# Kernel optimization log

Hardware: AMD Instinct MI355X
Metric: run time of the kernel (lower is better)

Reference implementation:

```python
import jax, jax.numpy as jnp
import numpy as np

TEMP_DIV = 13.0  # forward hard-codes attn / 13 (self.temperature is unused)


def setup_inputs() -> dict:
    key = jax.random.key(0)
    k1, k2, k3 = jax.random.split(key, 3)
    B, Lq, Lk, D = 8, 2048, 2048, 640
    q = jax.random.normal(k1, (B, Lq, D), dtype=jnp.float32)
    k = jax.random.normal(k2, (B, Lk, D), dtype=jnp.float32)
    v = jax.random.normal(k3, (B, Lk, D), dtype=jnp.float32)
    return {"q": q, "k": k, "v": v}


def _l2_scores(q, k):
    # -sum((q[:,:,None,:] - k[:,None,:,:])**2, axis=3) via the GEMM expansion
    # ||q||^2 - 2 q.k + ||k||^2  -> avoids the (B,Lq,Lk,D) intermediate.
    qq = jnp.sum(q * q, axis=-1)            # (B, Lq)
    kk = jnp.sum(k * k, axis=-1)            # (B, Lk)
    qk = jnp.einsum('bqd,bkd->bqk', q, k)   # (B, Lq, Lk)
    return -(qq[:, :, None] - 2.0 * qk + kk[:, None, :])


def reference(q, k, v):
    attn_logits = _l2_scores(q, k) / TEMP_DIV          # (B, Lq, Lk)
    log_attn = jax.nn.log_softmax(attn_logits, axis=2)
    attn = jnp.exp(log_attn)                            # softmax, shares the stable pass
    # dropout is identity in eval mode
    output = jnp.einsum('bqk,bkd->bqd', attn, v)        # bmm
    return (output, attn, log_attn)
```

## Files before the change

kernel.cpp:

```cpp
#include <hip/hip_runtime.h>


#define B_   8
#define LQ   2048
#define LK   2048
#define DD   640

typedef short s16x8 __attribute__((ext_vector_type(8)));
typedef float f32x4 __attribute__((ext_vector_type(4)));

__device__ __forceinline__ unsigned short f2bf(float x) {
    unsigned int u = __float_as_uint(x);
    unsigned int r = (u + 0x7fffu + ((u >> 16) & 1u)) >> 16;
    return (unsigned short)r;
}

__global__ __launch_bounds__(256) void cvt_norm2(const float* __restrict__ q,
                                                 const float* __restrict__ k,
                                                 unsigned short* __restrict__ q16,
                                                 unsigned short* __restrict__ k16,
                                                 float* __restrict__ qq,
                                                 float* __restrict__ kkn) {
    int row  = blockIdx.x * 4 + (threadIdx.x >> 6);
    int lane = threadIdx.x & 63;
    const float* src;
    unsigned short* dst;
    float* nrm;
    int r;
    if (row < B_ * LQ) { src = q; dst = q16; nrm = qq;  r = row; }
    else               { src = k; dst = k16; nrm = kkn; r = row - B_ * LQ; }
    const float4* s = (const float4*)(src + (size_t)r * DD);
    unsigned short* d = dst + (size_t)r * DD;
    float ss = 0.f;
    for (int t = lane; t < DD / 4; t += 64) {
        float4 x = s[t];
        ss += x.x * x.x + x.y * x.y + x.z * x.z + x.w * x.w;
        ushort4 o;
        o.x = f2bf(x.x); o.y = f2bf(x.y); o.z = f2bf(x.z); o.w = f2bf(x.w);
        *(ushort4*)(d + t * 4) = o;
    }
    #pragma unroll
    for (int o = 32; o; o >>= 1) ss += __shfl_xor(ss, o);
    if (lane == 0) nrm[r] = ss;
}

__global__ __launch_bounds__(256) void cvt_transpose_v(const float* __restrict__ v,
                                                       unsigned short* __restrict__ vt) {
    __shared__ float tile[64][65];
    int bx = blockIdx.x;
    int b  = bx / 320;
    int r  = bx % 320;
    int tj = r / 10;
    int td = r % 10;
    const float* src = v + (size_t)b * LK * DD + (size_t)tj * 64 * DD + td * 64;
    for (int e = threadIdx.x; e < 4096; e += 256) {
        int rr = e >> 6, cc = e & 63;
        tile[rr][cc] = src[(size_t)rr * DD + cc];
    }
    __syncthreads();
    unsigned short* dst = vt + (size_t)b * DD * LK + (size_t)td * 64 * LK + tj * 64;
    for (int e = threadIdx.x; e < 4096; e += 256) {
        int rr = e >> 6, cc = e & 63;
        dst[(size_t)rr * LK + cc] = f2bf(tile[cc][rr]);
    }
}

template <int LDA, int LDB, int KSZ, int NTN, int BCOLS, bool EPI>
__global__ __launch_bounds__(512, 2) void gemm8p(
    const unsigned short* __restrict__ A, const unsigned short* __restrict__ Bm,
    float* __restrict__ C, size_t strideA, size_t strideB, size_t strideC, int ldc,
    const float* __restrict__ qq, const float* __restrict__ kkn) {

    constexpr int KT = KSZ / 64;

    __shared__ unsigned short lA[2 * 16384];
    __shared__ unsigned short lB[2 * 16384];
    __shared__ float snm[512];

    int bx = blockIdx.x;
    int tm = bx & 7;
    int i  = bx >> 3;
    int tn = i % NTN;
    int b  = i / NTN;

    const unsigned short* Ab = A  + b * strideA + (size_t)tm * 256 * LDA;
    const unsigned short* Bb = Bm + b * strideB + (size_t)tn * 256 * LDB;

    int tid  = threadIdx.x;
    int w    = tid >> 6;
    int lane = tid & 63;
    int lrow = lane & 15;
    int lk4  = lane >> 4;
    int wm   = w >> 2;
    int wn   = w & 3;

    int bmax = BCOLS - tn * 256; if (bmax > 256) bmax = 256;

    if constexpr (EPI) {
        snm[tid] = (tid < 256) ? qq[b * LQ + tm * 256 + tid]
                               : kkn[b * LK + tn * 256 + (tid - 256)];
    }
    asm volatile("" ::: "memory");

    auto stage_chunk = [&](const unsigned short* Gb, int ldg, int rmax,
                           unsigned short* Lb, int kt, int s) {
        int row = ((s & 1) << 7) | (tid >> 2);
        int kh  = s >> 1;
        int ch  = tid & 3;
        int gr  = row < rmax ? row : rmax - 1;
        int sc  = kt * 64 + kh * 32 + ((ch ^ ((row >> 1) & 3)) << 3);
        __builtin_amdgcn_global_load_lds(
            (const __attribute__((address_space(1))) void*)(Gb + (size_t)gr * ldg + sc),
            (__attribute__((address_space(3))) void*)(Lb + s * 4096 + w * 512),
            16, 0, 0);
    };

    #pragma unroll
    for (int s = 0; s < 4; ++s) stage_chunk(Ab, LDA, 256,  lA,         0, s);
    #pragma unroll
    for (int s = 0; s < 4; ++s) stage_chunk(Bb, LDB, bmax, lB,         0, s);
    #pragma unroll
    for (int s = 0; s < 4; ++s) stage_chunk(Ab, LDA, 256,  lA + 16384, 1, s);
    #pragma unroll
    for (int s = 0; s < 4; ++s) stage_chunk(Bb, LDB, bmax, lB + 16384, 1, s);

    f32x4 acc[8][4] = {};

    auto bar = [&]() {
        __builtin_amdgcn_sched_barrier(0);
        asm volatile("" ::: "memory");
        __builtin_amdgcn_s_barrier();
        asm volatile("" ::: "memory");
        __builtin_amdgcn_sched_barrier(0);
    };

    auto run_iter = [&](int t, bool st) {
        int p = t & 1;
        const unsigned short* pA = lA + p * 16384;
        const unsigned short* pB = lB + p * 16384;
        unsigned short* sA = lA + p * 16384;
        unsigned short* sB = lB + p * 16384;
        int t2 = t + 2;
        s16x8 bf[4][2];
        #pragma unroll
        for (int j = 0; j < 4; ++j) {
            if (j == 0) {
                #pragma unroll
                for (int n = 0; n < 4; ++n)
                    #pragma unroll
                    for (int kh = 0; kh < 2; ++kh) {
                        int br = wn * 64 + n * 16 + lrow;
                        bf[n][kh] = *(const s16x8*)(pB + kh * 8192 + br * 32 +
                                                    ((lk4 ^ ((br >> 1) & 3)) << 3));
                    }
            }
            s16x8 af[2][2];
            #pragma unroll
            for (int m = 0; m < 2; ++m)
                #pragma unroll
                for (int kh = 0; kh < 2; ++kh) {
                    int ar = wm * 128 + (j * 2 + m) * 16 + lrow;
                    af[m][kh] = *(const s16x8*)(pA + kh * 8192 + ar * 32 +
                                                ((lk4 ^ ((ar >> 1) & 3)) << 3));
                }
            if (st) {
                if (j == 1) { stage_chunk(Bb, LDB, bmax, sB, t2, 0);
                              stage_chunk(Bb, LDB, bmax, sB, t2, 1); }
                if (j == 2) { stage_chunk(Bb, LDB, bmax, sB, t2, 2);
                              stage_chunk(Bb, LDB, bmax, sB, t2, 3); }
            }
            bar();
            __builtin_amdgcn_s_setprio(1);
            #pragma unroll
            for (int kh = 0; kh < 2; ++kh)
                #pragma unroll
                for (int m = 0; m < 2; ++m)
                    #pragma unroll
                    for (int n = 0; n < 4; ++n)
                        acc[j * 2 + m][n] = __builtin_amdgcn_mfma_f32_16x16x32_bf16(
                            af[m][kh], bf[n][kh], acc[j * 2 + m][n], 0, 0, 0);
            __builtin_amdgcn_s_setprio(0);
            bar();
        }
        if (st) {
            #pragma unroll
            for (int s = 0; s < 4; ++s) stage_chunk(Ab, LDA, 256, sA, t2, s);
        }
    };

    for (int t = 0; t < KT - 1; ++t) {
        asm volatile("s_waitcnt vmcnt(8)" ::: "memory");
        bar();
        run_iter(t, t + 2 < KT);
    }
    asm volatile("s_waitcnt vmcnt(0)" ::: "memory");
    bar();
    run_iter(KT - 1, false);

    float* Cb = C + b * strideC + (size_t)(tm * 256) * ldc + tn * 256;
    #pragma unroll
    for (int mi = 0; mi < 8; ++mi) {
        int rb = wm * 128 + mi * 16 + lk4 * 4;
        #pragma unroll
        for (int ni = 0; ni < 4; ++ni) {
            int col = wn * 64 + ni * 16 + lrow;
            if (col < bmax) {
                #pragma unroll
                for (int rr = 0; rr < 4; ++rr) {
                    float val = acc[mi][ni][rr];
                    if constexpr (EPI)
                        val = (2.0f * val - snm[rb + rr] - snm[256 + col]) * (1.0f / 13.0f);
                    Cb[(size_t)(rb + rr) * ldc + col] = val;
                }
            }
        }
    }
}

__global__ __launch_bounds__(256) void softmax_fix(float* __restrict__ logits,
                                                   float* __restrict__ attn,
                                                   unsigned short* __restrict__ a16) {
    __shared__ float redm[4], reds[4];
    size_t row = blockIdx.x;
    float* Lr = logits + row * LK;
    int tid = threadIdx.x;
    float x[8];
    *(float4*)(x)     = *(const float4*)(Lr + tid * 8);
    *(float4*)(x + 4) = *(const float4*)(Lr + tid * 8 + 4);

    float m = x[0];
    #pragma unroll
    for (int i = 1; i < 8; ++i) m = fmaxf(m, x[i]);
    #pragma unroll
    for (int o = 32; o; o >>= 1) m = fmaxf(m, __shfl_xor(m, o));
    int wv = tid >> 6, ln = tid & 63;
    if (ln == 0) redm[wv] = m;
    __syncthreads();
    m = fmaxf(fmaxf(redm[0], redm[1]), fmaxf(redm[2], redm[3]));

    float e[8];
    float s = 0.f;
    #pragma unroll
    for (int i = 0; i < 8; ++i) { e[i] = __expf(x[i] - m); s += e[i]; }
    #pragma unroll
    for (int o = 32; o; o >>= 1) s += __shfl_xor(s, o);
    if (ln == 0) reds[wv] = s;
    __syncthreads();
    s = reds[0] + reds[1] + reds[2] + reds[3];

    float lse = __logf(s);
    float inv = 1.0f / s;
    float at[8], la[8];
    #pragma unroll
    for (int i = 0; i < 8; ++i) { at[i] = e[i] * inv; la[i] = x[i] - m - lse; }

    float* Ar = attn + row * LK;
    *(float4*)(Ar + tid * 8)     = *(float4*)at;
    *(float4*)(Ar + tid * 8 + 4) = *(float4*)(at + 4);
    *(float4*)(Lr + tid * 8)     = *(float4*)la;
    *(float4*)(Lr + tid * 8 + 4) = *(float4*)(la + 4);

    unsigned short h[8];
    #pragma unroll
    for (int i = 0; i < 8; ++i) h[i] = f2bf(at[i]);
    unsigned short* Hr = a16 + row * LK;
    *(ushort4*)(Hr + tid * 8)     = *(ushort4*)h;
    *(ushort4*)(Hr + tid * 8 + 4) = *(ushort4*)(h + 4);
}

extern "C" void kernel_launch(void* const* d_in, const int* in_sizes, int n_in,
                              void* d_out, int out_size, void* d_ws, size_t ws_size,
                              hipStream_t stream) {
    const float* q = (const float*)d_in[0];
    const float* k = (const float*)d_in[1];
    const float* v = (const float*)d_in[2];

    float* out   = (float*)d_out;
    float* attn  = out + (size_t)B_ * LQ * DD;
    float* logat = attn + (size_t)B_ * LQ * LK;

    unsigned short* q16  = (unsigned short*)d_ws;
    unsigned short* k16  = q16 + (size_t)B_ * LQ * DD;
    unsigned short* v16t = k16 + (size_t)B_ * LK * DD;
    unsigned short* a16  = v16t + (size_t)B_ * DD * LK;
    float* qq  = (float*)(a16 + (size_t)B_ * LQ * LK);
    float* kkn = qq + (size_t)B_ * LQ;

    cvt_norm2<<<2 * B_ * LQ / 4, 256, 0, stream>>>(q, k, q16, k16, qq, kkn);
    cvt_transpose_v<<<B_ * (LK / 64) * (DD / 64), 256, 0, stream>>>(v, v16t);

    gemm8p<DD, DD, DD, 8, LK, true><<<B_ * 8 * 8, 512, 0, stream>>>(
        q16, k16, logat,
        (size_t)LQ * DD, (size_t)LK * DD, (size_t)LQ * LK, LK, qq, kkn);

    softmax_fix<<<B_ * LQ, 256, 0, stream>>>(logat, attn, a16);

    gemm8p<LK, LK, LK, 3, DD, false><<<B_ * 3 * 8, 512, 0, stream>>>(
        a16, v16t, out,
        (size_t)LQ * LK, (size_t)DD * LK, (size_t)LQ * DD, DD, nullptr, nullptr);
}
```

Baseline: 611.0 us.

## Add dedicated PV GEMM with 256x160 tiles and fuse conversion kernels

Replaces the generic second GEMM (attn @ V), which used 256-wide N tiles over D=640 and so had partial tiles and only 192 blocks, with a specialized kernel using 256x160 tiles. That gives 256 blocks with no wasted columns, a batch-staggered M index for L2 locality, and adjusted double-buffered LDS staging. It also merges the q/k conversion and the V transpose kernels into one launch to save a launch and let them overlap. The tradeoff is a smaller per-block tile, with 4x5 MFMA fragments per wave, which may lower arithmetic intensity.

New measurement: 595.9 us. -2.5%, faster.

```diff
diff --git a/kernel.cpp b/kernel.cpp
--- a/kernel.cpp
+++ b/kernel.cpp
@@ -15,53 +15,55 @@
     return (unsigned short)r;
 }
 
-__global__ __launch_bounds__(256) void cvt_norm2(const float* __restrict__ q,
-                                                 const float* __restrict__ k,
-                                                 unsigned short* __restrict__ q16,
-                                                 unsigned short* __restrict__ k16,
-                                                 float* __restrict__ qq,
-                                                 float* __restrict__ kkn) {
-    int row  = blockIdx.x * 4 + (threadIdx.x >> 6);
-    int lane = threadIdx.x & 63;
-    const float* src;
-    unsigned short* dst;
-    float* nrm;
-    int r;
-    if (row < B_ * LQ) { src = q; dst = q16; nrm = qq;  r = row; }
-    else               { src = k; dst = k16; nrm = kkn; r = row - B_ * LQ; }
-    const float4* s = (const float4*)(src + (size_t)r * DD);
-    unsigned short* d = dst + (size_t)r * DD;
-    float ss = 0.f;
-    for (int t = lane; t < DD / 4; t += 64) {
-        float4 x = s[t];
-        ss += x.x * x.x + x.y * x.y + x.z * x.z + x.w * x.w;
-        ushort4 o;
-        o.x = f2bf(x.x); o.y = f2bf(x.y); o.z = f2bf(x.z); o.w = f2bf(x.w);
-        *(ushort4*)(d + t * 4) = o;
-    }
-    #pragma unroll
-    for (int o = 32; o; o >>= 1) ss += __shfl_xor(ss, o);
-    if (lane == 0) nrm[r] = ss;
-}
-
-__global__ __launch_bounds__(256) void cvt_transpose_v(const float* __restrict__ v,
-                                                       unsigned short* __restrict__ vt) {
+__global__ __launch_bounds__(256) void cvt_all(const float* __restrict__ q,
+                                               const float* __restrict__ k,
+                                               const float* __restrict__ v,
+                                               unsigned short* __restrict__ q16,
+                                               unsigned short* __restrict__ k16,
+                                               unsigned short* __restrict__ vt,
+                                               float* __restrict__ qq,
+                                               float* __restrict__ kkn) {
     __shared__ float tile[64][65];
     int bx = blockIdx.x;
-    int b  = bx / 320;
-    int r  = bx % 320;
-    int tj = r / 10;
-    int td = r % 10;
-    const float* src = v + (size_t)b * LK * DD + (size_t)tj * 64 * DD + td * 64;
-    for (int e = threadIdx.x; e < 4096; e += 256) {
-        int rr = e >> 6, cc = e & 63;
-        tile[rr][cc] = src[(size_t)rr * DD + cc];
-    }
-    __syncthreads();
-    unsigned short* dst = vt + (size_t)b * DD * LK + (size_t)td * 64 * LK + tj * 64;
-    for (int e = threadIdx.x; e < 4096; e += 256) {
-        int rr = e >> 6, cc = e & 63;
-        dst[(size_t)rr * LK + cc] = f2bf(tile[cc][rr]);
+    if (bx < 8192) {
+        int row  = bx * 4 + (threadIdx.x >> 6);
+        int lane = threadIdx.x & 63;
+        const float* src;
+        unsigned short* dst;
+        float* nrm;
+        int r;
+        if (row < B_ * LQ) { src = q; dst = q16; nrm = qq;  r = row; }
+        else               { src = k; dst = k16; nrm = kkn; r = row - B_ * LQ; }
+        const float4* s = (const float4*)(src + (size_t)r * DD);
+        unsigned short* d = dst + (size_t)r * DD;
+        float ss = 0.f;
+        for (int t = lane; t < DD / 4; t += 64) {
+            float4 x = s[t];
+            ss += x.x * x.x + x.y * x.y + x.z * x.z + x.w * x.w;
+            ushort4 o;
+            o.x = f2bf(x.x); o.y = f2bf(x.y); o.z = f2bf(x.z); o.w = f2bf(x.w);
+            *(ushort4*)(d + t * 4) = o;
+        }
+        #pragma unroll
+        for (int o = 32; o; o >>= 1) ss += __shfl_xor(ss, o);
+        if (lane == 0) nrm[r] = ss;
+    } else {
+        int r0 = bx - 8192;
+        int b  = r0 / 320;
+        int r  = r0 % 320;
+        int tj = r / 10;
+        int td = r % 10;
+        const float* src = v + (size_t)b * LK * DD + (size_t)tj * 64 * DD + td * 64;
+        for (int e = threadIdx.x; e < 4096; e += 256) {
+            int rr = e >> 6, cc = e & 63;
+            tile[rr][cc] = src[(size_t)rr * DD + cc];
+        }
+        __syncthreads();
+        unsigned short* dst = vt + (size_t)b * DD * LK + (size_t)td * 64 * LK + tj * 64;
+        for (int e = threadIdx.x; e < 4096; e += 256) {
+            int rr = e >> 6, cc = e & 63;
+            dst[(size_t)rr * LK + cc] = f2bf(tile[cc][rr]);
+        }
     }
 }
 
@@ -217,6 +219,145 @@
     }
 }
 
+__global__ __launch_bounds__(512, 2) void gemm_pv(
+    const unsigned short* __restrict__ A, const unsigned short* __restrict__ Bm,
+    float* __restrict__ C) {
+
+    constexpr int KT = LK / 64;
+
+    __shared__ unsigned short lA[2 * 16384];
+    __shared__ unsigned short lB[2 * 12288];
+
+    int bx = blockIdx.x;
+    int x  = bx & 7;
+    int r  = bx >> 3;
+    int b  = r >> 2;
+    int tn = r & 3;
+    int tm = (x - b) & 7;
+
+    const unsigned short* Ab = A  + (size_t)b * LQ * LK + (size_t)tm * 256 * LK;
+    const unsigned short* Bb = Bm + (size_t)b * DD * LK + (size_t)tn * 160 * LK;
+
+    int tid  = threadIdx.x;
+    int w    = tid >> 6;
+    int lane = tid & 63;
+    int lrow = lane & 15;
+    int lk4  = lane >> 4;
+    int wm   = w >> 1;
+    int wn   = w & 1;
+
+    auto stageA = [&](int kt, int p, int s) {
+        int row = ((s & 1) << 7) | (tid >> 2);
+        int kh  = s >> 1;
+        int ch  = tid & 3;
+        int sc  = kt * 64 + kh * 32 + ((ch ^ ((row >> 1) & 3)) << 3);
+        __builtin_amdgcn_global_load_lds(
+            (const __attribute__((address_space(1))) void*)(Ab + (size_t)row * LK + sc),
+            (__attribute__((address_space(3))) void*)(lA + p * 16384 + s * 4096 + w * 512),
+            16, 0, 0);
+    };
+    auto stageB = [&](int kt, int p, int s) {
+        int g   = s * 512 + tid;
+        int kh  = g >= 768;
+        int rem = g - kh * 768;
+        int row = rem >> 2;
+        int ch  = rem & 3;
+        int gr  = row < 160 ? row : 159;
+        int sc  = kt * 64 + kh * 32 + ((ch ^ ((row >> 1) & 3)) << 3);
+        __builtin_amdgcn_global_load_lds(
+            (const __attribute__((address_space(1))) void*)(Bb + (size_t)gr * LK + sc),
+            (__attribute__((address_space(3))) void*)(lB + p * 12288 + s * 4096 + w * 512),
+            16, 0, 0);
+    };
+
+    #pragma unroll
+    for (int s = 0; s < 4; ++s) stageA(0, 0, s);
+    #pragma unroll
+    for (int s = 0; s < 3; ++s) stageB(0, 0, s);
+    #pragma unroll
+    for (int s = 0; s < 4; ++s) stageA(1, 1, s);
+    #pragma unroll
+    for (int s = 0; s < 3; ++s) stageB(1, 1, s);
+
+    f32x4 acc[4][5] = {};
+
+    auto bar = [&]() {
+        __builtin_amdgcn_sched_barrier(0);
+        asm volatile("" ::: "memory");
+        __builtin_amdgcn_s_barrier();
+        asm volatile("" ::: "memory");
+        __builtin_amdgcn_sched_barrier(0);
+    };
+
+    auto run_iter = [&](int t, bool st) {
+        int p = t & 1;
+        const unsigned short* pA = lA + p * 16384;
+        const unsigned short* pB = lB + p * 12288;
+        int t2 = t + 2;
+        s16x8 bf[5][2];
+        #pragma unroll
+        for (int j = 0; j < 4; ++j) {
+            if (j == 0) {
+                #pragma unroll
+                for (int n = 0; n < 5; ++n)
+                    #pragma unroll
+                    for (int kh = 0; kh < 2; ++kh) {
+                        int br = wn * 80 + n * 16 + lrow;
+                        bf[n][kh] = *(const s16x8*)(pB + kh * 6144 + br * 32 +
+                                                    ((lk4 ^ ((br >> 1) & 3)) << 3));
+                    }
+            }
+            s16x8 af[2];
+            #pragma unroll
+            for (int kh = 0; kh < 2; ++kh) {
+                int ar = wm * 64 + j * 16 + lrow;
+                af[kh] = *(const s16x8*)(pA + kh * 8192 + ar * 32 +
+                                         ((lk4 ^ ((ar >> 1) & 3)) << 3));
+            }
+            if (st) {
+                if (j == 1) { stageB(t2, p, 0); stageB(t2, p, 1); }
+                if (j == 2) { stageB(t2, p, 2); }
+            }
+            bar();
+            __builtin_amdgcn_s_setprio(1);
+            #pragma unroll
+            for (int kh = 0; kh < 2; ++kh)
+                #pragma unroll
+                for (int n = 0; n < 5; ++n)
+                    acc[j][n] = __builtin_amdgcn_mfma_f32_16x16x32_bf16(
+                        af[kh], bf[n][kh], acc[j][n], 0, 0, 0);
+            __builtin_amdgcn_s_setprio(0);
+            bar();
+        }
+        if (st) {
+            #pragma unroll
+            for (int s = 0; s < 4; ++s) stageA(t2, p, s);
+        }
+    };
+
+    for (int t = 0; t < KT - 1; ++t) {
+        asm volatile("s_waitcnt vmcnt(7)" ::: "memory");
+        bar();
+        run_iter(t, t + 2 < KT);
+    }
+    asm volatile("s_waitcnt vmcnt(0)" ::: "memory");
+    bar();
+    run_iter(KT - 1, false);
+
+    float* Cb = C + (size_t)b * LQ * DD + (size_t)(tm * 256) * DD + tn * 160;
+    #pragma unroll
+    for (int mi = 0; mi < 4; ++mi) {
+        int rb = wm * 64 + mi * 16 + lk4 * 4;
+        #pragma unroll
+        for (int ni = 0; ni < 5; ++ni) {
+            int col = wn * 80 + ni * 16 + lrow;
+            #pragma unroll
+            for (int rr = 0; rr < 4; ++rr)
+                Cb[(size_t)(rb + rr) * DD + col] = acc[mi][ni][rr];
+        }
+    }
+}
+
 __global__ __launch_bounds__(256) void softmax_fix(float* __restrict__ logits,
                                                    float* __restrict__ attn,
                                                    unsigned short* __restrict__ a16) {
@@ -286,8 +427,8 @@
     float* qq  = (float*)(a16 + (size_t)B_ * LQ * LK);
     float* kkn = qq + (size_t)B_ * LQ;
 
-    cvt_norm2<<<2 * B_ * LQ / 4, 256, 0, stream>>>(q, k, q16, k16, qq, kkn);
-    cvt_transpose_v<<<B_ * (LK / 64) * (DD / 64), 256, 0, stream>>>(v, v16t);
+    cvt_all<<<8192 + B_ * (LK / 64) * (DD / 64), 256, 0, stream>>>(
+        q, k, v, q16, k16, v16t, qq, kkn);
 
     gemm8p<DD, DD, DD, 8, LK, true><<<B_ * 8 * 8, 512, 0, stream>>>(
         q16, k16, logat,
@@ -295,7 +436,5 @@
 
     softmax_fix<<<B_ * LQ, 256, 0, stream>>>(logat, attn, a16);
 
-    gemm8p<LK, LK, LK, 3, DD, false><<<B_ * 3 * 8, 512, 0, stream>>>(
-        a16, v16t, out,
-        (size_t)LQ * LK, (size_t)DD * LK, (size_t)LQ * DD, DD, nullptr, nullptr);
-}
+    gemm_pv<<<B_ * 8 * 4, 512, 0, stream>>>(a16, v16t, out);
+}
```
